# Performance work log

Measured on AMD Instinct MI355X. Metric: run time of the kernel, lower is better.

The kernel has to match this reference:

```python
import jax, jax.numpy as jnp
import numpy as np

N_LAYERS = 6
D_T = 6144   # d_transcoder (features per layer)
D_M = 768    # d_model (residual stream)
TOK = 128    # tokens (batch*seq)


def setup_inputs() -> dict:
    key = jax.random.key(0)
    k_x, k_enc, k_dec = jax.random.split(key, 3)
    x = jax.random.normal(k_x, (N_LAYERS, TOK, D_M), jnp.float32)
    W_enc = jax.random.normal(k_enc, (N_LAYERS, D_T, D_M), jnp.float32) * 0.02
    b_enc = jnp.zeros((N_LAYERS, D_T), jnp.float32)
    b_dec = jnp.zeros((N_LAYERS, D_M), jnp.float32)
    # Padded cross-layer decoder: W_dec[i, j] is the decoder from features at
    # layer i writing into layer j's MLP output; only j >= i is valid
    # (original stores a ragged list of [d_transcoder, n_layers - i, d_model]).
    W_dec = jax.random.normal(k_dec, (N_LAYERS, N_LAYERS, D_T, D_M), jnp.float32) * 0.02
    dec_mask = jnp.triu(jnp.ones((N_LAYERS, N_LAYERS), dtype=bool))  # mask[i, j] = (j >= i)
    W_dec = jnp.where(dec_mask[:, :, None, None], W_dec, 0.0)
    return {"x": x, "W_enc": W_enc, "b_enc": b_enc, "b_dec": b_dec,
            "W_dec": W_dec, "dec_mask": dec_mask}


def reference(x, W_enc, b_enc, b_dec, W_dec, dec_mask):
    # Encode: per-layer feature activations [n_layers, tok, d_transcoder]
    acts = jax.nn.relu(jnp.einsum('lnd,lfd->lnf', x, W_enc) + b_enc[:, None, :])
    # Decode: layer-i features write to all layers j >= i (mask enforces triangle)
    Wd = jnp.where(dec_mask[:, :, None, None], W_dec, 0.0)
    recon = jnp.einsum('inf,ijfd->jnd', acts, Wd) + b_dec[:, None, :]
    return recon  # [n_layers, tok, d_model]
```

## Files before the change

kernel.cpp:

```cpp
#include <hip/hip_runtime.h>
#include <hip/hip_bf16.h>

#define NL 6
#define DT 6144
#define DM 768
#define TOK 128

#define EF 32
#define EK 256
#define ENST (DM / EK)
#define NVE (2 * ENST)

#define TD 256
#define NTD 3
#define FC 768
#define NFC 8
#define NSTEP (FC / 32)
#define TILE_ELEMS (TOK * TD)

using bf16x8 = __attribute__((ext_vector_type(8))) short;
using f32x4  = __attribute__((ext_vector_type(4))) float;

typedef unsigned int u32;
typedef __attribute__((address_space(1))) const u32 gu32;
typedef __attribute__((address_space(3))) u32 lu32;

__device__ __forceinline__ void stage16(const float* g, float* l) {
  __builtin_amdgcn_global_load_lds((gu32*)g, (lu32*)l, 16, 0, 0);
}

__device__ __forceinline__ short f2bf(float f) {
  union { float f; unsigned u; } c; c.f = f;
  unsigned u = c.u;
  u += 0x7fffu + ((u >> 16) & 1u);
  return (short)(u >> 16);
}

__device__ __forceinline__ float bf2f(ushort u) {
  union { unsigned u; float f; } c; c.u = ((unsigned)u) << 16;
  return c.f;
}

__global__ void initcvt_k(const float* __restrict__ b_dec,
                          const float* __restrict__ x,
                          float* __restrict__ out, ushort* __restrict__ xb) {
  int idx = blockIdx.x * 256 + threadIdx.x;
  if (idx < NL * TOK * DM) {
    out[idx] = b_dec[(idx / (TOK * DM)) * DM + (idx % DM)];
    xb[idx] = (ushort)f2bf(x[idx]);
  }
}

__global__ __launch_bounds__(256, 2) void encode_k(
    const ushort* __restrict__ xb, const float* __restrict__ W_enc,
    const float* __restrict__ b_enc, ushort* __restrict__ acts)
{
  __shared__ float lw[2][EF][EK];

  const int l  = blockIdx.x / 96;
  const int fp = (blockIdx.x % 96) * 64;
  const int w    = threadIdx.x >> 6;
  const int lane = threadIdx.x & 63;
  const int lo = lane & 15, hi = lane >> 4;

  const float*  We = W_enc + ((size_t)l * DT + fp) * DM;
  const ushort* Xb = xb + (size_t)l * TOK * DM;

  f32x4 acc[2][2];
  #pragma unroll
  for (int mi = 0; mi < 2; ++mi)
    #pragma unroll
    for (int ni = 0; ni < 2; ++ni)
      acc[mi][ni] = f32x4{0.f, 0.f, 0.f, 0.f};

  #pragma unroll
  for (int q = 0; q < 8; ++q) {
    const int row = w * 8 + q;
    stage16(We + (size_t)row * DM + (lane ^ (row & 7)) * 4, &lw[0][row][0]);
  }
  __syncthreads();

  int cur = 0;
  #pragma unroll 1
  for (int v = 0; v < NVE; ++v) {
    const int tt = v / ENST;
    const int st = v % ENST;

    if (v + 1 < NVE) {
      const int tt2 = (v + 1) / ENST;
      const int st2 = (v + 1) % ENST;
      #pragma unroll
      for (int q = 0; q < 8; ++q) {
        const int row = w * 8 + q;
        stage16(We + (size_t)(tt2 * EF + row) * DM + st2 * EK + (lane ^ (row & 7)) * 4,
                &lw[cur ^ 1][row][0]);
      }
    }

    const int sw = lo & 7;
    #pragma unroll
    for (int ks = 0; ks < EK / 32; ++ks) {
      bf16x8 a[2], b[2];
      #pragma unroll
      for (int mi = 0; mi < 2; ++mi)
        a[mi] = *(const bf16x8*)(Xb + (size_t)(w * 32 + mi * 16 + lo) * DM
                                 + st * EK + ks * 32 + hi * 8);
      #pragma unroll
      for (int ni = 0; ni < 2; ++ni) {
        const int c0 = (ks * 8 + hi * 2) ^ sw;
        const int c1 = (ks * 8 + hi * 2 + 1) ^ sw;
        const float4 b0 = *(const float4*)&lw[cur][ni * 16 + lo][c0 * 4];
        const float4 b1 = *(const float4*)&lw[cur][ni * 16 + lo][c1 * 4];
        b[ni][0] = f2bf(b0.x); b[ni][1] = f2bf(b0.y);
        b[ni][2] = f2bf(b0.z); b[ni][3] = f2bf(b0.w);
        b[ni][4] = f2bf(b1.x); b[ni][5] = f2bf(b1.y);
        b[ni][6] = f2bf(b1.z); b[ni][7] = f2bf(b1.w);
      }

      #pragma unroll
      for (int mi = 0; mi < 2; ++mi)
        #pragma unroll
        for (int ni = 0; ni < 2; ++ni)
          acc[mi][ni] = __builtin_amdgcn_mfma_f32_16x16x32_bf16(a[mi], b[ni], acc[mi][ni], 0, 0, 0);
    }

    if (st == ENST - 1) {
      #pragma unroll
      for (int ni = 0; ni < 2; ++ni) {
        const int f = fp + tt * EF + ni * 16 + lo;
        const float bias = b_enc[l * DT + f];
        #pragma unroll
        for (int mi = 0; mi < 2; ++mi) {
          #pragma unroll
          for (int rr = 0; rr < 4; ++rr) {
            const int n = w * 32 + mi * 16 + hi * 4 + rr;
            float vv = acc[mi][ni][rr] + bias;
            vv = vv > 0.f ? vv : 0.f;
            acts[((size_t)l * TOK + n) * DT + f] = (ushort)f2bf(vv);
            acc[mi][ni][rr] = 0.f;
          }
        }
      }
    }

    __syncthreads();
    cur ^= 1;
  }
}

__device__ const int PI_[21]  = {0,0,0,0,0,0, 1,1,1,1,1, 2,2,2,2, 3,3,3, 4,4, 5};
__device__ const int PJ_[21]  = {0,1,2,3,4,5, 1,2,3,4,5, 2,3,4,5, 3,4,5, 4,5, 5};
__device__ const int OFFI_[6] = {0, 6, 11, 15, 18, 20};

__global__ __launch_bounds__(512, 4) void decode_part_k(
    const ushort* __restrict__ acts, const float* __restrict__ W_dec,
    ushort* __restrict__ part)
{
  __shared__ float lw[2][32][TD];

  const int bid = blockIdx.x;
  const int p  = bid / (NFC * NTD);
  const int rm = bid % (NFC * NTD);
  const int c  = rm / NTD;
  const int t  = rm % NTD;
  const int i = PI_[p], j = PJ_[p];
  const int w    = threadIdx.x >> 6;
  const int mw   = w >> 2;
  const int dwv  = w & 3;
  const int lane = threadIdx.x & 63;
  const int lo = lane & 15, hi = lane >> 4;
  const int fb = c * FC;
  const int m0 = mw * 64;
  (void)j;

  const float*  Wb = W_dec + ((size_t)(i * NL + j) * DT + fb) * DM + t * TD;
  const ushort* Ab = acts + (size_t)i * TOK * DT + fb;

  f32x4 acc[4][4];
  #pragma unroll
  for (int mi = 0; mi < 4; ++mi)
    #pragma unroll
    for (int ni = 0; ni < 4; ++ni)
      acc[mi][ni] = f32x4{0.f, 0.f, 0.f, 0.f};

  #pragma unroll
  for (int q = 0; q < 4; ++q) {
    const int row = w * 4 + q;
    stage16(Wb + (size_t)row * DM + lane * 4, &lw[0][row][0]);
  }
  __syncthreads();

  int cur = 0;
  #pragma unroll 1
  for (int s = 0; s < NSTEP; ++s) {
    if (s + 1 < NSTEP) {
      const float* Ws = Wb + (size_t)(s + 1) * 32 * DM;
      #pragma unroll
      for (int q = 0; q < 4; ++q) {
        const int row = w * 4 + q;
        stage16(Ws + (size_t)row * DM + lane * 4, &lw[cur ^ 1][row][0]);
      }
    }

    bf16x8 a[4];
    #pragma unroll
    for (int mi = 0; mi < 4; ++mi)
      a[mi] = *(const bf16x8*)(Ab + (size_t)(m0 + mi * 16 + lo) * DT + s * 32 + hi * 8);

    bf16x8 bb[4];
    #pragma unroll
    for (int ni = 0; ni < 4; ++ni) {
      const int col = dwv * 64 + ni * 16 + lo;
      #pragma unroll
      for (int e = 0; e < 8; ++e)
        bb[ni][e] = f2bf(lw[cur][hi * 8 + e][col]);
    }

    #pragma unroll
    for (int mi = 0; mi < 4; ++mi)
      #pragma unroll
      for (int ni = 0; ni < 4; ++ni)
        acc[mi][ni] = __builtin_amdgcn_mfma_f32_16x16x32_bf16(a[mi], bb[ni], acc[mi][ni], 0, 0, 0);

    __syncthreads();
    cur ^= 1;
  }

  ushort* pp = part + (size_t)bid * TILE_ELEMS;
  #pragma unroll
  for (int ni = 0; ni < 4; ++ni) {
    const int dl = dwv * 64 + ni * 16 + lo;
    #pragma unroll
    for (int mi = 0; mi < 4; ++mi)
      #pragma unroll
      for (int rr = 0; rr < 4; ++rr)
        pp[(size_t)(m0 + mi * 16 + hi * 4 + rr) * TD + dl] = (ushort)f2bf(acc[mi][ni][rr]);
  }
}

__global__ void reduce_k(const ushort* __restrict__ part,
                         const float* __restrict__ b_dec,
                         float* __restrict__ out)
{
  const int idx = blockIdx.x * 256 + threadIdx.x;
  if (idx >= NL * TOK * DM) return;
  const int j   = idx / (TOK * DM);
  const int rem = idx % (TOK * DM);
  const int n   = rem / DM;
  const int d   = rem % DM;
  const int t   = d >> 8;
  const int dl  = d & (TD - 1);

  float s = b_dec[j * DM + d];
  for (int i = 0; i <= j; ++i) {
    const int p = OFFI_[i] + (j - i);
    const ushort* pb = part + ((size_t)(p * NFC) * NTD + t) * TILE_ELEMS
                       + (size_t)n * TD + dl;
    #pragma unroll
    for (int c = 0; c < NFC; ++c)
      s += bf2f(pb[(size_t)c * NTD * TILE_ELEMS]);
  }
  out[idx] = s;
}

__global__ __launch_bounds__(256, 2) void decode_atomic_k(
    const ushort* __restrict__ acts, const float* __restrict__ W_dec,
    float* __restrict__ out)
{
  __shared__ float lw[2][32][TD];

  const int bid = blockIdx.x;
  const int p  = bid / (NTD * NFC);
  const int rm = bid % (NTD * NFC);
  const int c  = rm / NTD;
  const int t  = rm % NTD;
  const int i = PI_[p], j = PJ_[p];
  const int w = threadIdx.x >> 6;
  const int lane = threadIdx.x & 63;
  const int lo = lane & 15, hi = lane >> 4;
  const int fb = c * FC;

  const float*  Wb = W_dec + ((size_t)(i * NL + j) * DT + fb) * DM + t * TD;
  const ushort* Ab = acts + (size_t)i * TOK * DT + fb;

  f32x4 acc[8][4];
  #pragma unroll
  for (int mi = 0; mi < 8; ++mi)
    #pragma unroll
    for (int ni = 0; ni < 4; ++ni)
      acc[mi][ni] = f32x4{0.f, 0.f, 0.f, 0.f};

  #pragma unroll
  for (int q = 0; q < 8; ++q) {
    const int row = w * 8 + q;
    stage16(Wb + (size_t)row * DM + lane * 4, &lw[0][row][0]);
  }
  __syncthreads();

  int cur = 0;
  #pragma unroll 1
  for (int s = 0; s < NSTEP; ++s) {
    if (s + 1 < NSTEP) {
      const float* Ws = Wb + (size_t)(s + 1) * 32 * DM;
      #pragma unroll
      for (int q = 0; q < 8; ++q) {
        const int row = w * 8 + q;
        stage16(Ws + (size_t)row * DM + lane * 4, &lw[cur ^ 1][row][0]);
      }
    }

    bf16x8 a[8];
    #pragma unroll
    for (int mi = 0; mi < 8; ++mi)
      a[mi] = *(const bf16x8*)(Ab + (size_t)(mi * 16 + lo) * DT + s * 32 + hi * 8);

    bf16x8 bb[4];
    #pragma unroll
    for (int ni = 0; ni < 4; ++ni) {
      const int col = w * 64 + ni * 16 + lo;
      #pragma unroll
      for (int e = 0; e < 8; ++e)
        bb[ni][e] = f2bf(lw[cur][hi * 8 + e][col]);
    }

    #pragma unroll
    for (int mi = 0; mi < 8; ++mi)
      #pragma unroll
      for (int ni = 0; ni < 4; ++ni)
        acc[mi][ni] = __builtin_amdgcn_mfma_f32_16x16x32_bf16(a[mi], bb[ni], acc[mi][ni], 0, 0, 0);

    __syncthreads();
    cur ^= 1;
  }

  float* oj = out + (size_t)j * TOK * DM;
  #pragma unroll
  for (int ni = 0; ni < 4; ++ni) {
    const int d = t * TD + w * 64 + ni * 16 + lo;
    #pragma unroll
    for (int mi = 0; mi < 8; ++mi)
      #pragma unroll
      for (int rr = 0; rr < 4; ++rr)
        atomicAdd(oj + (size_t)(mi * 16 + hi * 4 + rr) * DM + d, acc[mi][ni][rr]);
  }
}

extern "C" void kernel_launch(void* const* d_in, const int* in_sizes, int n_in,
                              void* d_out, int out_size, void* d_ws, size_t ws_size,
                              hipStream_t stream) {
  const float* x     = (const float*)d_in[0];
  const float* W_enc = (const float*)d_in[1];
  const float* b_enc = (const float*)d_in[2];
  const float* b_dec = (const float*)d_in[3];
  const float* W_dec = (const float*)d_in[4];
  float* out = (float*)d_out;

  const size_t actsB = (size_t)NL * TOK * DT * 2;
  const size_t xbB   = (size_t)NL * TOK * DM * 2;
  const size_t partB = (size_t)21 * NFC * NTD * TILE_ELEMS * 2;

  ushort* acts = (ushort*)d_ws;
  ushort* xb   = (ushort*)((char*)d_ws + actsB);
  ushort* part = (ushort*)((char*)d_ws + actsB + xbB);

  initcvt_k<<<dim3((NL * TOK * DM + 255) / 256), dim3(256), 0, stream>>>(b_dec, x, out, xb);
  encode_k<<<dim3(NL * 96), dim3(256), 0, stream>>>(xb, W_enc, b_enc, acts);

  if (ws_size >= actsB + xbB + partB) {
    decode_part_k<<<dim3(21 * NFC * NTD), dim3(512), 0, stream>>>(acts, W_dec, part);
    reduce_k<<<dim3((NL * TOK * DM + 255) / 256), dim3(256), 0, stream>>>(part, b_dec, out);
  } else {
    decode_atomic_k<<<dim3(21 * NFC * NTD), dim3(256), 0, stream>>>(acts, W_dec, out);
  }
}
```

Before: 182.8 us.

## Retile decode to full-width 1024-thread blocks and vectorize partial reduction

The decode kernel now gives each block the full 768-wide output row instead of a 256-column slice. Blocks use 1024 threads and step through K in chunks of 16, with half the lanes feeding zeros into the 32-wide MFMA. The feature dimension is split 12 ways, so there are fewer, larger blocks, and activation tiles are no longer reloaded across column slices. The reduce kernel reads 8 bf16 values per thread as vectors. The cost is that half of the MFMA work is wasted, the grid is much smaller (252 blocks), and the partial-sum buffer is larger.

```diff
diff --git a/kernel.cpp b/kernel.cpp
--- a/kernel.cpp
+++ b/kernel.cpp
@@ -11,12 +11,16 @@
 #define ENST (DM / EK)
 #define NVE (2 * ENST)
 
-#define TD 256
-#define NTD 3
-#define FC 768
-#define NFC 8
-#define NSTEP (FC / 32)
-#define TILE_ELEMS (TOK * TD)
+#define NFCD 12
+#define FCD (DT / NFCD)
+#define NSTEPD (FCD / 16)
+#define PT (TOK * DM)
+
+#define TDA 256
+#define NTDA 3
+#define FCA 768
+#define NFCA 8
+#define NSTEPA (FCA / 32)
 
 using bf16x8 = __attribute__((ext_vector_type(8))) short;
 using f32x4  = __attribute__((ext_vector_type(4))) float;
@@ -152,89 +156,91 @@
 __device__ const int PJ_[21]  = {0,1,2,3,4,5, 1,2,3,4,5, 2,3,4,5, 3,4,5, 4,5, 5};
 __device__ const int OFFI_[6] = {0, 6, 11, 15, 18, 20};
 
-__global__ __launch_bounds__(512, 4) void decode_part_k(
+__global__ __launch_bounds__(1024, 4) void decode_part_k(
     const ushort* __restrict__ acts, const float* __restrict__ W_dec,
     ushort* __restrict__ part)
 {
-  __shared__ float lw[2][32][TD];
+  __shared__ float lw[2][16][DM];
 
   const int bid = blockIdx.x;
-  const int p  = bid / (NFC * NTD);
-  const int rm = bid % (NFC * NTD);
-  const int c  = rm / NTD;
-  const int t  = rm % NTD;
+  const int p = bid / NFCD, c = bid % NFCD;
   const int i = PI_[p], j = PJ_[p];
   const int w    = threadIdx.x >> 6;
-  const int mw   = w >> 2;
-  const int dwv  = w & 3;
+  const int mw   = w >> 3;
+  const int dw   = w & 7;
   const int lane = threadIdx.x & 63;
   const int lo = lane & 15, hi = lane >> 4;
-  const int fb = c * FC;
+  const int fb = c * FCD;
   const int m0 = mw * 64;
-  (void)j;
-
-  const float*  Wb = W_dec + ((size_t)(i * NL + j) * DT + fb) * DM + t * TD;
+  const int n0 = dw * 96;
+  const int khalf = (hi < 2) ? 1 : 0;
+
+  const float*  Wb = W_dec + ((size_t)(i * NL + j) * DT + fb) * DM;
   const ushort* Ab = acts + (size_t)i * TOK * DT + fb;
 
-  f32x4 acc[4][4];
+  f32x4 acc[4][6];
   #pragma unroll
   for (int mi = 0; mi < 4; ++mi)
     #pragma unroll
-    for (int ni = 0; ni < 4; ++ni)
+    for (int ni = 0; ni < 6; ++ni)
       acc[mi][ni] = f32x4{0.f, 0.f, 0.f, 0.f};
 
   #pragma unroll
-  for (int q = 0; q < 4; ++q) {
-    const int row = w * 4 + q;
-    stage16(Wb + (size_t)row * DM + lane * 4, &lw[0][row][0]);
-  }
+  for (int q = 0; q < 3; ++q)
+    stage16(Wb + (size_t)w * DM + q * 256 + lane * 4, &lw[0][w][q * 256]);
   __syncthreads();
 
   int cur = 0;
   #pragma unroll 1
-  for (int s = 0; s < NSTEP; ++s) {
-    if (s + 1 < NSTEP) {
-      const float* Ws = Wb + (size_t)(s + 1) * 32 * DM;
-      #pragma unroll
-      for (int q = 0; q < 4; ++q) {
-        const int row = w * 4 + q;
-        stage16(Ws + (size_t)row * DM + lane * 4, &lw[cur ^ 1][row][0]);
-      }
-    }
-
-    bf16x8 a[4];
-    #pragma unroll
-    for (int mi = 0; mi < 4; ++mi)
-      a[mi] = *(const bf16x8*)(Ab + (size_t)(m0 + mi * 16 + lo) * DT + s * 32 + hi * 8);
-
-    bf16x8 bb[4];
-    #pragma unroll
-    for (int ni = 0; ni < 4; ++ni) {
-      const int col = dwv * 64 + ni * 16 + lo;
-      #pragma unroll
-      for (int e = 0; e < 8; ++e)
-        bb[ni][e] = f2bf(lw[cur][hi * 8 + e][col]);
-    }
-
-    #pragma unroll
-    for (int mi = 0; mi < 4; ++mi)
-      #pragma unroll
-      for (int ni = 0; ni < 4; ++ni)
-        acc[mi][ni] = __builtin_amdgcn_mfma_f32_16x16x32_bf16(a[mi], bb[ni], acc[mi][ni], 0, 0, 0);
+  for (int s = 0; s < NSTEPD; ++s) {
+    if (s + 1 < NSTEPD) {
+      const float* Ws = Wb + (size_t)((s + 1) * 16 + w) * DM;
+      #pragma unroll
+      for (int q = 0; q < 3; ++q)
+        stage16(Ws + q * 256 + lane * 4, &lw[cur ^ 1][w][q * 256]);
+    }
+
+    const int ka = khalf ? (s * 16 + hi * 8) : 0;
+    #pragma unroll
+    for (int mh = 0; mh < 2; ++mh) {
+      bf16x8 a[2];
+      #pragma unroll
+      for (int u = 0; u < 2; ++u) {
+        const int tok = m0 + (mh * 2 + u) * 16 + lo;
+        bf16x8 av = *(const bf16x8*)(Ab + (size_t)tok * DT + ka);
+        #pragma unroll
+        for (int e = 0; e < 8; ++e) a[u][e] = khalf ? av[e] : (short)0;
+      }
+      #pragma unroll
+      for (int ni = 0; ni < 6; ++ni) {
+        const int col = n0 + ni * 16 + lo;
+        bf16x8 b;
+        #pragma unroll
+        for (int e = 0; e < 8; ++e) {
+          const int row = khalf ? (hi * 8 + e) : 0;
+          const float v = lw[cur][row][col];
+          b[e] = khalf ? f2bf(v) : (short)0;
+        }
+        #pragma unroll
+        for (int u = 0; u < 2; ++u)
+          acc[mh * 2 + u][ni] = __builtin_amdgcn_mfma_f32_16x16x32_bf16(
+              a[u], b, acc[mh * 2 + u][ni], 0, 0, 0);
+      }
+    }
 
     __syncthreads();
     cur ^= 1;
   }
 
-  ushort* pp = part + (size_t)bid * TILE_ELEMS;
-  #pragma unroll
-  for (int ni = 0; ni < 4; ++ni) {
-    const int dl = dwv * 64 + ni * 16 + lo;
+  ushort* pp = part + (size_t)bid * PT;
+  #pragma unroll
+  for (int ni = 0; ni < 6; ++ni) {
+    const int d = n0 + ni * 16 + lo;
     #pragma unroll
     for (int mi = 0; mi < 4; ++mi)
       #pragma unroll
       for (int rr = 0; rr < 4; ++rr)
-        pp[(size_t)(m0 + mi * 16 + hi * 4 + rr) * TD + dl] = (ushort)f2bf(acc[mi][ni][rr]);
+        pp[(size_t)(m0 + mi * 16 + hi * 4 + rr) * DM + d] = (ushort)f2bf(acc[mi][ni][rr]);
   }
 }
 
@@ -242,45 +248,49 @@
                          const float* __restrict__ b_dec,
                          float* __restrict__ out)
 {
-  const int idx = blockIdx.x * 256 + threadIdx.x;
-  if (idx >= NL * TOK * DM) return;
+  const int t8 = blockIdx.x * 256 + threadIdx.x;
+  if (t8 >= NL * TOK * DM / 8) return;
+  const int idx = t8 * 8;
   const int j   = idx / (TOK * DM);
   const int rem = idx % (TOK * DM);
-  const int n   = rem / DM;
-  const int d   = rem % DM;
-  const int t   = d >> 8;
-  const int dl  = d & (TD - 1);
-
-  float s = b_dec[j * DM + d];
+  const int dd  = rem % DM;
+
+  float s[8];
+  #pragma unroll
+  for (int e = 0; e < 8; ++e) s[e] = b_dec[j * DM + dd + e];
+
   for (int i = 0; i <= j; ++i) {
     const int p = OFFI_[i] + (j - i);
-    const ushort* pb = part + ((size_t)(p * NFC) * NTD + t) * TILE_ELEMS
-                       + (size_t)n * TD + dl;
-    #pragma unroll
-    for (int c = 0; c < NFC; ++c)
-      s += bf2f(pb[(size_t)c * NTD * TILE_ELEMS]);
-  }
-  out[idx] = s;
+    const ushort* pb = part + (size_t)p * NFCD * PT + rem;
+    #pragma unroll
+    for (int c = 0; c < NFCD; ++c) {
+      bf16x8 v = *(const bf16x8*)(pb + (size_t)c * PT);
+      #pragma unroll
+      for (int e = 0; e < 8; ++e) s[e] += bf2f((ushort)v[e]);
+    }
+  }
+  #pragma unroll
+  for (int e = 0; e < 8; ++e) out[idx + e] = s[e];
 }
 
 __global__ __launch_bounds__(256, 2) void decode_atomic_k(
     const ushort* __restrict__ acts, const float* __restrict__ W_dec,
     float* __restrict__ out)
 {
-  __shared__ float lw[2][32][TD];
+  __shared__ float lw[2][32][TDA];
 
   const int bid = blockIdx.x;
-  const int p  = bid / (NTD * NFC);
-  const int rm = bid % (NTD * NFC);
-  const int c  = rm / NTD;
-  const int t  = rm % NTD;
+  const int p  = bid / (NTDA * NFCA);
+  const int rm = bid % (NTDA * NFCA);
+  const int c  = rm / NTDA;
+  const int t  = rm % NTDA;
   const int i = PI_[p], j = PJ_[p];
   const int w = threadIdx.x >> 6;
   const int lane = threadIdx.x & 63;
   const int lo = lane & 15, hi = lane >> 4;
-  const int fb = c * FC;
-
-  const float*  Wb = W_dec + ((size_t)(i * NL + j) * DT + fb) * DM + t * TD;
+  const int fb = c * FCA;
+
+  const float*  Wb = W_dec + ((size_t)(i * NL + j) * DT + fb) * DM + t * TDA;
   const ushort* Ab = acts + (size_t)i * TOK * DT + fb;
 
   f32x4 acc[8][4];
@@ -299,8 +309,8 @@
 
   int cur = 0;
   #pragma unroll 1
-  for (int s = 0; s < NSTEP; ++s) {
-    if (s + 1 < NSTEP) {
+  for (int s = 0; s < NSTEPA; ++s) {
+    if (s + 1 < NSTEPA) {
       const float* Ws = Wb + (size_t)(s + 1) * 32 * DM;
       #pragma unroll
       for (int q = 0; q < 8; ++q) {
@@ -336,7 +346,7 @@
   float* oj = out + (size_t)j * TOK * DM;
   #pragma unroll
   for (int ni = 0; ni < 4; ++ni) {
-    const int d = t * TD + w * 64 + ni * 16 + lo;
+    const int d = t * TDA + w * 64 + ni * 16 + lo;
     #pragma unroll
     for (int mi = 0; mi < 8; ++mi)
       #pragma unroll
@@ -357,7 +367,7 @@
 
   const size_t actsB = (size_t)NL * TOK * DT * 2;
   const size_t xbB   = (size_t)NL * TOK * DM * 2;
-  const size_t partB = (size_t)21 * NFC * NTD * TILE_ELEMS * 2;
+  const size_t partB = (size_t)21 * NFCD * PT * 2;
 
   ushort* acts = (ushort*)d_ws;
   ushort* xb   = (ushort*)((char*)d_ws + actsB);
@@ -367,9 +377,9 @@
   encode_k<<<dim3(NL * 96), dim3(256), 0, stream>>>(xb, W_enc, b_enc, acts);
 
   if (ws_size >= actsB + xbB + partB) {
-    decode_part_k<<<dim3(21 * NFC * NTD), dim3(512), 0, stream>>>(acts, W_dec, part);
-    reduce_k<<<dim3((NL * TOK * DM + 255) / 256), dim3(256), 0, stream>>>(part, b_dec, out);
+    decode_part_k<<<dim3(21 * NFCD), dim3(1024), 0, stream>>>(acts, W_dec, part);
+    reduce_k<<<dim3((NL * TOK * DM / 8 + 255) / 256), dim3(256), 0, stream>>>(part, b_dec, out);
   } else {
-    decode_atomic_k<<<dim3(21 * NFC * NTD), dim3(256), 0, stream>>>(acts, W_dec, out);
-  }
-}
+    decode_atomic_k<<<dim3(21 * NFCA * NTDA), dim3(256), 0, stream>>>(acts, W_dec, out);
+  }
+}
```

Result: slower. 361.8 us (+98.0%).
